# Kernel optimization log

Measured on AMD Instinct MI355X. Metric: run time of the kernel, lower is better.

Reference implementation:

```python
import jax, jax.numpy as jnp
import numpy as np

B, S, D, E, TOPK = 8, 4096, 1024, 64, 2
TEMP = 0.01


def setup_inputs() -> dict:
    key = jax.random.key(0)
    k_x, k_w1, k_b1, k_w2, k_b2 = jax.random.split(key, 5)
    x = jax.random.normal(k_x, (B, S, D), dtype=jnp.float32)
    # torch.nn.Linear default init ~ U(-1/sqrt(fan_in), 1/sqrt(fan_in)); scale ok for reference
    W1 = jax.random.normal(k_w1, (D, 2 * D), dtype=jnp.float32) * (1.0 / np.sqrt(D))
    b1 = jax.random.normal(k_b1, (2 * D,), dtype=jnp.float32) * 0.01
    W2 = jax.random.normal(k_w2, (2 * D, E), dtype=jnp.float32) * (1.0 / np.sqrt(2 * D))
    b2 = jax.random.normal(k_b2, (E,), dtype=jnp.float32) * 0.01
    return {"x": x, "W1": W1, "b1": b1, "W2": W2, "b2": b2}


def reference(x, W1, b1, W2, b2):
    # 2-layer MLP router: [B,S,D] -> [B,S,2D] -> [B,S,E]
    h = jax.nn.relu(jnp.einsum('bsd,df->bsf', x, W1) + b1)
    logits = jnp.einsum('bsf,fe->bse', h, W2) + b2
    # top-k over experts
    top_k_logits, indices = jax.lax.top_k(logits, TOPK)  # [B,S,K]
    # scatter top-k logits into a -inf-filled tensor: equivalent to masking,
    # since scattered values equal logits at those positions
    keep = jax.nn.one_hot(indices, E, dtype=bool).any(axis=-2)  # [B,S,E]
    sparse_logits = jnp.where(keep, logits, -jnp.inf)
    router_output = jax.nn.softmax(sparse_logits, axis=-1)
    ori_router_output = jax.nn.softmax(logits / TEMP, axis=-1)
    return (ori_router_output, router_output, indices)
```

## Files before the change

kernel.cpp:

```cpp
#include <hip/hip_runtime.h>
#include <math.h>
#include <stdint.h>

#define M_TOK 32768
#define D_IN  1024
#define F_HID 2048
#define E_EXP 64

#define O_ORI 0
#define O_RTR (M_TOK * E_EXP)
#define O_IDX (2 * M_TOK * E_EXP)

typedef _Float16 half8 __attribute__((ext_vector_type(8)));
typedef float    f32x4 __attribute__((ext_vector_type(4)));
typedef unsigned int uint32;
typedef uint32   u32x4 __attribute__((ext_vector_type(4)));

#define WS_XH  ((size_t)0)
#define WS_XL  (WS_XH  + (size_t)M_TOK * D_IN * 2)
#define WS_W1H (WS_XL  + (size_t)M_TOK * D_IN * 2)
#define WS_W1L (WS_W1H + (size_t)D_IN * F_HID * 2)
#define WS_W2H (WS_W1L + (size_t)D_IN * F_HID * 2)
#define WS_W2L (WS_W2H + (size_t)F_HID * E_EXP * 2)
#define WS_P   (WS_W2L + (size_t)F_HID * E_EXP * 2)
#define WS_NEED_FULL (WS_P + (size_t)8 * M_TOK * E_EXP * 4)

__device__ __forceinline__ void split_sc(float v, float sc, unsigned short& h, unsigned short& l) {
    const _Float16 hh = (_Float16)v;
    const float hf = (float)hh;
    const _Float16 hs = (_Float16)(hf * sc);
    const _Float16 ls = (_Float16)((v - hf) * sc);
    h = __builtin_bit_cast(unsigned short, hs);
    l = __builtin_bit_cast(unsigned short, ls);
}


__global__ void split_x_k(const float* __restrict__ x,
                          unsigned short* __restrict__ xh, unsigned short* __restrict__ xl) {
    size_t i = ((size_t)blockIdx.x * 256 + threadIdx.x) * 4;
    const float4 v = *(const float4*)&x[i];
    ushort4 h, l;
    split_sc(v.x, 64.f, h.x, l.x); split_sc(v.y, 64.f, h.y, l.y);
    split_sc(v.z, 64.f, h.z, l.z); split_sc(v.w, 64.f, h.w, l.w);
    *(ushort4*)&xh[i] = h;
    *(ushort4*)&xl[i] = l;
}

__global__ void split_w1t_k(const float* __restrict__ W1,
                            unsigned short* __restrict__ wh, unsigned short* __restrict__ wl) {
    __shared__ float t[32][33];
    const int d0 = blockIdx.x * 32;
    const int f0 = blockIdx.y * 32;
    const int r  = threadIdx.x >> 3;
    const int c4 = (threadIdx.x & 7) * 4;
    const float4 v = *(const float4*)&W1[(size_t)(d0 + r) * F_HID + f0 + c4];
    t[r][c4 + 0] = v.x; t[r][c4 + 1] = v.y; t[r][c4 + 2] = v.z; t[r][c4 + 3] = v.w;
    __syncthreads();
    ushort4 h, l;
    split_sc(t[c4 + 0][r], 64.f, h.x, l.x);
    split_sc(t[c4 + 1][r], 64.f, h.y, l.y);
    split_sc(t[c4 + 2][r], 64.f, h.z, l.z);
    split_sc(t[c4 + 3][r], 64.f, h.w, l.w);
    *(ushort4*)&wh[(size_t)(f0 + r) * D_IN + d0 + c4] = h;
    *(ushort4*)&wl[(size_t)(f0 + r) * D_IN + d0 + c4] = l;
}

__global__ void split_w2f_k(const float* __restrict__ W2,
                            unsigned short* __restrict__ wh, unsigned short* __restrict__ wl) {
    const int s  = blockIdx.x;
    const int nt = threadIdx.x >> 6;
    const int l  = threadIdx.x & 63;
    const int fb = s * 32 + (l >> 4) * 8;
    const int e  = nt * 16 + (l & 15);
    unsigned short h[8], lo[8];
#pragma unroll
    for (int j = 0; j < 8; ++j)
        split_sc(W2[(size_t)(fb + j) * E_EXP + e], 16.f, h[j], lo[j]);
    const size_t base = ((size_t)(s * 4 + nt) * 64 + l) * 8;
#pragma unroll
    for (int j = 0; j < 4; ++j) {
        ((ushort4*)&wh[base])[0] = make_ushort4(h[0], h[1], h[2], h[3]);
        ((ushort4*)&wh[base])[1] = make_ushort4(h[4], h[5], h[6], h[7]);
        ((ushort4*)&wl[base])[0] = make_ushort4(lo[0], lo[1], lo[2], lo[3]);
        ((ushort4*)&wl[base])[1] = make_ushort4(lo[4], lo[5], lo[6], lo[7]);
    }
}


__device__ __forceinline__ uint32 swz(uint32 o) { return o ^ (((o >> 7) & 7u) << 4); }

#define STAGE16(SRCP, DSTP) \
    __builtin_amdgcn_global_load_lds((const __attribute__((address_space(1))) void*)(SRCP), \
                                     (__attribute__((address_space(3))) void*)(DSTP), 16, 0, 0)


__launch_bounds__(512, 2)
__global__ void gemm1_8w(const unsigned short* __restrict__ xh, const unsigned short* __restrict__ xl,
                         const unsigned short* __restrict__ w1h, const unsigned short* __restrict__ w1l,
                         const unsigned short* __restrict__ w2fh, const unsigned short* __restrict__ w2fl,
                         const float* __restrict__ b1,
                         float* __restrict__ partials)
{
    __shared__ __align__(16) unsigned char lds[131072];

    const int tid  = threadIdx.x;
    const int lane = tid & 63;
    const int w    = tid >> 6;
    const int c15  = lane & 15;
    const int g    = lane >> 4;
    const int wr   = w >> 2;
    const int wc   = w & 3;

    const int bid  = blockIdx.x;
    const int fblk = bid & 7;
    const int mblk = bid >> 3;
    const size_t tok0 = (size_t)mblk * 128;
    const int f0 = fblk * 256;

    uint32 arow, ahalf, brow[2], bhalf[2];
    {
        const uint32 sA = swz((uint32)(w * 1024 + lane * 16));
        arow = sA >> 6; ahalf = (sA & 63u) >> 1;
#pragma unroll
        for (int j = 0; j < 2; ++j) {
            const uint32 sB = swz((uint32)(j * 8192 + w * 1024 + lane * 16));
            brow[j] = sB >> 6; bhalf[j] = (sB & 63u) >> 1;
        }
    }

    uint32 offA[4], offB[4];
#pragma unroll
    for (int m = 0; m < 4; ++m)
        offA[m] = swz((uint32)((wr * 64 + m * 16 + c15) * 64 + g * 16));
#pragma unroll
    for (int n = 0; n < 4; ++n)
        offB[n] = swz((uint32)((wc * 64 + n * 16 + c15) * 64 + g * 16));

    f32x4 acc[4][4];
#pragma unroll
    for (int m = 0; m < 4; ++m)
#pragma unroll
        for (int n = 0; n < 4; ++n) acc[m][n] = (f32x4){0.f, 0.f, 0.f, 0.f};

#define STAGE_T(T, BUF) do {                                                         \
    const int d0_ = (T) * 32;                                                        \
    const size_t asrc = (tok0 + arow) * D_IN + (size_t)(d0_ + (int)ahalf);           \
    STAGE16(xh + asrc, lds + (BUF) * 16384 + w * 1024);                              \
    STAGE16(xl + asrc, lds + (BUF) * 16384 + 8192 + w * 1024);                       \
    _Pragma("unroll")                                                                \
    for (int j = 0; j < 2; ++j) {                                                    \
        const size_t bsrc = ((size_t)f0 + brow[j]) * D_IN + (size_t)(d0_ + (int)bhalf[j]); \
        STAGE16(w1h + bsrc, lds + 32768 + (BUF) * 32768 + j * 8192 + w * 1024);      \
        STAGE16(w1l + bsrc, lds + 32768 + (BUF) * 32768 + 16384 + j * 8192 + w * 1024); \
    } } while (0)

    STAGE_T(0, 0);
    STAGE_T(1, 1);

#pragma unroll 1
    for (int t = 0; t < 32; ++t) {
        if (t < 31) asm volatile("s_waitcnt vmcnt(6)" ::: "memory");
        else        asm volatile("s_waitcnt vmcnt(0)" ::: "memory");
        __builtin_amdgcn_s_barrier();
        const unsigned char* Ab = lds + (t & 1) * 16384;
        const unsigned char* Bb = lds + 32768 + (t & 1) * 32768;

        half8 b1f[4], b2f[4];
#pragma unroll
        for (int n = 0; n < 4; ++n) {
            b1f[n] = *(const half8*)(Bb + offB[n]);
            b2f[n] = *(const half8*)(Bb + 16384 + offB[n]);
        }
        half8 a1f[2], a2f[2];
#pragma unroll
        for (int m = 0; m < 2; ++m) {
            a1f[m] = *(const half8*)(Ab + offA[m]);
            a2f[m] = *(const half8*)(Ab + 8192 + offA[m]);
        }
        __builtin_amdgcn_s_setprio(1);
#pragma unroll
        for (int m = 0; m < 2; ++m)
#pragma unroll
            for (int n = 0; n < 4; ++n) {
                acc[m][n] = __builtin_amdgcn_mfma_f32_16x16x32_f16(a1f[m], b1f[n], acc[m][n], 0, 0, 0);
                acc[m][n] = __builtin_amdgcn_mfma_f32_16x16x32_f16(a1f[m], b2f[n], acc[m][n], 0, 0, 0);
                acc[m][n] = __builtin_amdgcn_mfma_f32_16x16x32_f16(a2f[m], b1f[n], acc[m][n], 0, 0, 0);
            }
        __builtin_amdgcn_s_setprio(0);
#pragma unroll
        for (int m = 0; m < 2; ++m) {
            a1f[m] = *(const half8*)(Ab + offA[2 + m]);
            a2f[m] = *(const half8*)(Ab + 8192 + offA[2 + m]);
        }
        __builtin_amdgcn_s_setprio(1);
#pragma unroll
        for (int m = 0; m < 2; ++m)
#pragma unroll
            for (int n = 0; n < 4; ++n) {
                acc[2 + m][n] = __builtin_amdgcn_mfma_f32_16x16x32_f16(a1f[m], b1f[n], acc[2 + m][n], 0, 0, 0);
                acc[2 + m][n] = __builtin_amdgcn_mfma_f32_16x16x32_f16(a1f[m], b2f[n], acc[2 + m][n], 0, 0, 0);
                acc[2 + m][n] = __builtin_amdgcn_mfma_f32_16x16x32_f16(a2f[m], b1f[n], acc[2 + m][n], 0, 0, 0);
            }
        __builtin_amdgcn_s_setprio(0);
        __builtin_amdgcn_s_barrier();
        if (t + 2 < 32) STAGE_T(t + 2, t & 1);
    }
#undef STAGE_T

    {
        float bv[4];
#pragma unroll
        for (int n = 0; n < 4; ++n) bv[n] = b1[f0 + wc * 64 + n * 16 + c15];
#pragma unroll
        for (int m = 0; m < 4; ++m)
#pragma unroll
            for (int n = 0; n < 4; ++n)
#pragma unroll
                for (int r = 0; r < 4; ++r) {
                    float hv = acc[m][n][r] * (1.f / 4096.f) + bv[n];
                    hv = fmaxf(hv, 0.f);
                    const _Float16 hh = (_Float16)hv;
                    const float hf = (float)hh;
                    const _Float16 hsv = (_Float16)(hf * 16.f);
                    const _Float16 lsv = (_Float16)((hv - hf) * 16.f);
                    const uint32 pk = (uint32)__builtin_bit_cast(unsigned short, hsv)
                                    | ((uint32)__builtin_bit_cast(unsigned short, lsv) << 16);
                    const int tok = wr * 64 + m * 16 + g * 4 + r;
                    const int fl  = wc * 64 + n * 16 + c15;
                    *(uint32*)(lds + tok * 1024 + ((fl * 4) ^ ((tok & 15) << 4))) = pk;
                }
    }
    __syncthreads();

    f32x4 acc2[4];
#pragma unroll
    for (int nt = 0; nt < 4; ++nt) acc2[nt] = (f32x4){0.f, 0.f, 0.f, 0.f};

    const int wtok0 = w * 16;
    const int tokA  = wtok0 + c15;
#pragma unroll
    for (int s = 0; s < 8; ++s) {
        const int kf = s * 32 + g * 8;
        const int sg = fblk * 8 + s;
        half8 bf1[4], bf2[4];
#pragma unroll
        for (int nt = 0; nt < 4; ++nt) {
            const size_t base = ((size_t)(sg * 4 + nt) * 64 + lane) * 8;
            bf1[nt] = *(const half8*)&w2fh[base];
            bf2[nt] = *(const half8*)&w2fl[base];
        }
        const u32x4 q0 = *(const u32x4*)(lds + tokA * 1024 + (((kf    ) * 4) ^ (c15 << 4)));
        const u32x4 q1 = *(const u32x4*)(lds + tokA * 1024 + (((kf + 4) * 4) ^ (c15 << 4)));
        u32x4 hi4, lo4;
        hi4[0] = __builtin_amdgcn_perm(q0[1], q0[0], 0x05040100u);
        hi4[1] = __builtin_amdgcn_perm(q0[3], q0[2], 0x05040100u);
        hi4[2] = __builtin_amdgcn_perm(q1[1], q1[0], 0x05040100u);
        hi4[3] = __builtin_amdgcn_perm(q1[3], q1[2], 0x05040100u);
        lo4[0] = __builtin_amdgcn_perm(q0[1], q0[0], 0x07060302u);
        lo4[1] = __builtin_amdgcn_perm(q0[3], q0[2], 0x07060302u);
        lo4[2] = __builtin_amdgcn_perm(q1[1], q1[0], 0x07060302u);
        lo4[3] = __builtin_amdgcn_perm(q1[3], q1[2], 0x07060302u);
        const half8 a1 = __builtin_bit_cast(half8, hi4);
        const half8 a2 = __builtin_bit_cast(half8, lo4);
#pragma unroll
        for (int nt = 0; nt < 4; ++nt) {
            acc2[nt] = __builtin_amdgcn_mfma_f32_16x16x32_f16(a1, bf1[nt], acc2[nt], 0, 0, 0);
            acc2[nt] = __builtin_amdgcn_mfma_f32_16x16x32_f16(a1, bf2[nt], acc2[nt], 0, 0, 0);
            acc2[nt] = __builtin_amdgcn_mfma_f32_16x16x32_f16(a2, bf1[nt], acc2[nt], 0, 0, 0);
        }
    }

    float* pout = partials + ((size_t)fblk * M_TOK + tok0) * E_EXP;
#pragma unroll
    for (int nt = 0; nt < 4; ++nt)
#pragma unroll
        for (int r = 0; r < 4; ++r) {
            const int tl = wtok0 + g * 4 + r;
            pout[(size_t)tl * E_EXP + nt * 16 + c15] = acc2[nt][r] * (1.f / 256.f);
        }
}


__launch_bounds__(256, 4)
__global__ void finalize(const float* __restrict__ partials,
                         const float* __restrict__ b2,
                         float* __restrict__ out)
{
    const int lane = threadIdx.x & 63;
    const int w    = threadIdx.x >> 6;
    const size_t tok0 = (size_t)blockIdx.x * 64;
    const int e = lane;
    const float be = b2[e];

#pragma unroll 1
    for (int i = 0; i < 16; ++i) {
        const size_t tok = tok0 + (size_t)w * 16 + i;
        float l = be;
#pragma unroll
        for (int p = 0; p < 8; ++p)
            l += partials[((size_t)p * M_TOK + tok) * E_EXP + e];

        float v = l; int idx = e;
#pragma unroll
        for (int m = 32; m >= 1; m >>= 1) {
            const float ov = __shfl_xor(v, m, 64);
            const int   oi = __shfl_xor(idx, m, 64);
            if (ov > v || (ov == v && oi < idx)) { v = ov; idx = oi; }
        }
        const float m1 = v; const int i1 = idx;

        v = (e == i1) ? -INFINITY : l; idx = e;
#pragma unroll
        for (int m = 32; m >= 1; m >>= 1) {
            const float ov = __shfl_xor(v, m, 64);
            const int   oi = __shfl_xor(idx, m, 64);
            if (ov > v || (ov == v && oi < idx)) { v = ov; idx = oi; }
        }
        const int i2 = idx;

        const float ex = expf((l - m1) * 100.0f);
        float s = ex;
#pragma unroll
        for (int m = 32; m >= 1; m >>= 1) s += __shfl_xor(s, m, 64);
        const float ori = ex / s;

        const float q = (e == i1 || e == i2) ? expf(l - m1) : 0.f;
        float s2 = q;
#pragma unroll
        for (int m = 32; m >= 1; m >>= 1) s2 += __shfl_xor(s2, m, 64);
        const float rtr = q / s2;

        out[O_ORI + tok * E_EXP + e] = ori;
        out[O_RTR + tok * E_EXP + e] = rtr;
        if (e == 0) {
            out[O_IDX + tok * 2 + 0] = (float)i1;
            out[O_IDX + tok * 2 + 1] = (float)i2;
        }
    }
}


#define BT  64
#define NB  256

__launch_bounds__(256, 2)
__global__ void router_mfma(const unsigned short* __restrict__ xh, const unsigned short* __restrict__ xl,
                            const unsigned short* __restrict__ w1h, const unsigned short* __restrict__ w1l,
                            const unsigned short* __restrict__ w2fh, const unsigned short* __restrict__ w2fl,
                            const float* __restrict__ b1, const float* __restrict__ b2,
                            float* __restrict__ out)
{
    __shared__ __align__(16) unsigned char xs_h[BT * 64];
    __shared__ __align__(16) unsigned char xs_l[BT * 64];
    __shared__ __align__(16) unsigned char w1s_h[NB * 64];
    __shared__ __align__(16) unsigned char w1s_l[NB * 64];
    __shared__ __align__(16) unsigned char hsbuf[BT * 132 * 4];

    const int tid  = threadIdx.x;
    const int lane = tid & 63;
    const int w    = tid >> 6;
    const int c15  = lane & 15;
    const int g    = lane >> 4;
    const size_t tok0 = (size_t)blockIdx.x * BT;

    uint32* hs = (uint32*)hsbuf;
    float*  ls = (float*)hsbuf;

    f32x4 acc2h[4], acc2x[4];
#pragma unroll
    for (int nt = 0; nt < 4; ++nt) {
        acc2h[nt] = (f32x4){0.f, 0.f, 0.f, 0.f};
        acc2x[nt] = (f32x4){0.f, 0.f, 0.f, 0.f};
    }

    const uint32 kqb = (uint32)g * 16u;

    for (int fc = 0; fc < F_HID; fc += NB) {
        f32x4 ahh[4][4], axx[4][4];
#pragma unroll
        for (int mt = 0; mt < 4; ++mt)
#pragma unroll
            for (int nt = 0; nt < 4; ++nt) {
                ahh[mt][nt] = (f32x4){0.f, 0.f, 0.f, 0.f};
                axx[mt][nt] = (f32x4){0.f, 0.f, 0.f, 0.f};
            }

        for (int d0 = 0; d0 < D_IN; d0 += 32) {
            __syncthreads();
            {
                uint32 o = (uint32)w * 1024u + (uint32)lane * 16u;
                uint32 s = swz(o);
                uint32 r = s >> 6, hb = (s & 63u) >> 1;
                const unsigned short* sp;
                sp = xh + (tok0 + r) * D_IN + (size_t)(d0 + (int)hb);
                STAGE16(sp, xs_h + (size_t)w * 1024);
                sp = xl + (tok0 + r) * D_IN + (size_t)(d0 + (int)hb);
                STAGE16(sp, xs_l + (size_t)w * 1024);
#pragma unroll
                for (int q = 0; q < 4; ++q) {
                    const uint32 c_ = (uint32)(q * 4 + w);
                    uint32 o2 = c_ * 1024u + (uint32)lane * 16u;
                    uint32 s2 = swz(o2);
                    uint32 r2 = s2 >> 6, hb2 = (s2 & 63u) >> 1;
                    sp = w1h + ((size_t)(fc + (int)r2)) * D_IN + (size_t)(d0 + (int)hb2);
                    STAGE16(sp, w1s_h + (size_t)c_ * 1024);
                    sp = w1l + ((size_t)(fc + (int)r2)) * D_IN + (size_t)(d0 + (int)hb2);
                    STAGE16(sp, w1s_l + (size_t)c_ * 1024);
                }
            }
            __syncthreads();

            half8 ah[4], al[4], bh[4], bl[4];
#pragma unroll
            for (int mt = 0; mt < 4; ++mt) {
                const uint32 off = swz((uint32)(mt * 16 + c15) * 64u + kqb);
                ah[mt] = *(const half8*)(xs_h + off);
                al[mt] = *(const half8*)(xs_l + off);
            }
#pragma unroll
            for (int nt = 0; nt < 4; ++nt) {
                const uint32 row = (uint32)(w * 64 + nt * 16 + c15);
                const uint32 off = swz(row * 64u + kqb);
                bh[nt] = *(const half8*)(w1s_h + off);
                bl[nt] = *(const half8*)(w1s_l + off);
            }
#pragma unroll
            for (int mt = 0; mt < 4; ++mt)
#pragma unroll
                for (int nt = 0; nt < 4; ++nt) {
                    ahh[mt][nt] = __builtin_amdgcn_mfma_f32_16x16x32_f16(ah[mt], bh[nt], ahh[mt][nt], 0, 0, 0);
                    axx[mt][nt] = __builtin_amdgcn_mfma_f32_16x16x32_f16(ah[mt], bl[nt], axx[mt][nt], 0, 0, 0);
                    axx[mt][nt] = __builtin_amdgcn_mfma_f32_16x16x32_f16(al[mt], bh[nt], axx[mt][nt], 0, 0, 0);
                }
        }

        const int fl0 = (w & 1) * 64;
#pragma unroll
        for (int phase = 0; phase < 2; ++phase) {
            if ((w >> 1) == phase) {
#pragma unroll
                for (int nt = 0; nt < 4; ++nt) {
                    const float b1v = b1[fc + w * 64 + nt * 16 + c15];
#pragma unroll
                    for (int mt = 0; mt < 4; ++mt) {
#pragma unroll
                        for (int r = 0; r < 4; ++r) {
                            float hv = (ahh[mt][nt][r] + axx[mt][nt][r]) * (1.f / 4096.f) + b1v;
                            hv = fmaxf(hv, 0.f);
                            const _Float16 hhv0 = (_Float16)hv;
                            const float hf = (float)hhv0;
                            const _Float16 hhv = (_Float16)(hf * 16.f);
                            const _Float16 hlv = (_Float16)((hv - hf) * 16.f);
                            uint32 pk = (uint32)__builtin_bit_cast(unsigned short, hhv)
                                      | ((uint32)__builtin_bit_cast(unsigned short, hlv) << 16);
                            const int t = mt * 16 + g * 4 + r;
                            hs[t * 132 + fl0 + nt * 16 + c15] = pk;
                        }
                    }
                }
            }
            __syncthreads();
            const int tA = w * 16 + c15;
#pragma unroll
            for (int ktl = 0; ktl < 4; ++ktl) {
                const u32x4 q0 = *(const u32x4*)&hs[tA * 132 + ktl * 32 + g * 8];
                const u32x4 q1 = *(const u32x4*)&hs[tA * 132 + ktl * 32 + g * 8 + 4];
                u32x4 hi4, lo4;
                hi4[0] = __builtin_amdgcn_perm(q0[1], q0[0], 0x05040100u);
                hi4[1] = __builtin_amdgcn_perm(q0[3], q0[2], 0x05040100u);
                hi4[2] = __builtin_amdgcn_perm(q1[1], q1[0], 0x05040100u);
                hi4[3] = __builtin_amdgcn_perm(q1[3], q1[2], 0x05040100u);
                lo4[0] = __builtin_amdgcn_perm(q0[1], q0[0], 0x07060302u);
                lo4[1] = __builtin_amdgcn_perm(q0[3], q0[2], 0x07060302u);
                lo4[2] = __builtin_amdgcn_perm(q1[1], q1[0], 0x07060302u);
                lo4[3] = __builtin_amdgcn_perm(q1[3], q1[2], 0x07060302u);
                const half8 a_h = __builtin_bit_cast(half8, hi4);
                const half8 a_l = __builtin_bit_cast(half8, lo4);
                const int sg = (fc >> 5) + phase * 4 + ktl;
#pragma unroll
                for (int nt = 0; nt < 4; ++nt) {
                    const size_t base = ((size_t)(sg * 4 + nt) * 64 + lane) * 8;
                    const half8 b_h = *(const half8*)&w2fh[base];
                    const half8 b_l = *(const half8*)&w2fl[base];
                    acc2h[nt] = __builtin_amdgcn_mfma_f32_16x16x32_f16(a_h, b_h, acc2h[nt], 0, 0, 0);
                    acc2x[nt] = __builtin_amdgcn_mfma_f32_16x16x32_f16(a_h, b_l, acc2x[nt], 0, 0, 0);
                    acc2x[nt] = __builtin_amdgcn_mfma_f32_16x16x32_f16(a_l, b_h, acc2x[nt], 0, 0, 0);
                }
            }
            __syncthreads();
        }
    }

#pragma unroll
    for (int nt = 0; nt < 4; ++nt)
#pragma unroll
        for (int r = 0; r < 4; ++r) {
            const int t = w * 16 + g * 4 + r;
            ls[t * 68 + nt * 16 + c15] = (acc2h[nt][r] + acc2x[nt][r]) * (1.f / 256.f);
        }
    __syncthreads();

    const int e = lane;
    const float be = b2[e];
#pragma unroll 1
    for (int i = 0; i < 16; ++i) {
        const float l = ls[(w * 16 + i) * 68 + e] + be;

        float v = l; int idx = e;
#pragma unroll
        for (int m = 32; m >= 1; m >>= 1) {
            const float ov = __shfl_xor(v, m, 64);
            const int   oi = __shfl_xor(idx, m, 64);
            if (ov > v || (ov == v && oi < idx)) { v = ov; idx = oi; }
        }
        const float m1 = v; const int i1 = idx;

        v = (e == i1) ? -INFINITY : l; idx = e;
#pragma unroll
        for (int m = 32; m >= 1; m >>= 1) {
            const float ov = __shfl_xor(v, m, 64);
            const int   oi = __shfl_xor(idx, m, 64);
            if (ov > v || (ov == v && oi < idx)) { v = ov; idx = oi; }
        }
        const int i2 = idx;

        const float ex = expf((l - m1) * 100.0f);
        float s = ex;
#pragma unroll
        for (int m = 32; m >= 1; m >>= 1) s += __shfl_xor(s, m, 64);
        const float ori = ex / s;

        const float q = (e == i1 || e == i2) ? expf(l - m1) : 0.f;
        float s2 = q;
#pragma unroll
        for (int m = 32; m >= 1; m >>= 1) s2 += __shfl_xor(s2, m, 64);
        const float rtr = q / s2;

        const size_t tok = tok0 + (size_t)w * 16 + i;
        out[O_ORI + tok * E_EXP + e] = ori;
        out[O_RTR + tok * E_EXP + e] = rtr;
        if (e == 0) {
            out[O_IDX + tok * 2 + 0] = (float)i1;
            out[O_IDX + tok * 2 + 1] = (float)i2;
        }
    }
}


extern "C" void kernel_launch(void* const* d_in, const int* in_sizes, int n_in,
                              void* d_out, int out_size, void* d_ws, size_t ws_size,
                              hipStream_t stream) {
    const float* x  = (const float*)d_in[0];
    const float* W1 = (const float*)d_in[1];
    const float* b1 = (const float*)d_in[2];
    const float* W2 = (const float*)d_in[3];
    const float* b2 = (const float*)d_in[4];
    float* out = (float*)d_out;

    unsigned char* ws = (unsigned char*)d_ws;
    unsigned short* xh  = (unsigned short*)(ws + WS_XH);
    unsigned short* xl  = (unsigned short*)(ws + WS_XL);
    unsigned short* w1h = (unsigned short*)(ws + WS_W1H);
    unsigned short* w1l = (unsigned short*)(ws + WS_W1L);
    unsigned short* w2h = (unsigned short*)(ws + WS_W2H);
    unsigned short* w2l = (unsigned short*)(ws + WS_W2L);
    float*          parts = (float*)(ws + WS_P);

    hipLaunchKernelGGL(split_x_k,  dim3(M_TOK * D_IN / 4 / 256), dim3(256), 0, stream, x, xh, xl);
    hipLaunchKernelGGL(split_w1t_k, dim3(D_IN / 32, F_HID / 32), dim3(256), 0, stream, W1, w1h, w1l);
    hipLaunchKernelGGL(split_w2f_k, dim3(F_HID / 32), dim3(256), 0, stream, W2, w2h, w2l);

    if (ws_size >= WS_NEED_FULL) {
        hipLaunchKernelGGL(gemm1_8w, dim3(2048), dim3(512), 0, stream,
                           xh, xl, w1h, w1l, w2h, w2l, b1, parts);
        hipLaunchKernelGGL(finalize, dim3(M_TOK / 64), dim3(256), 0, stream, parts, b2, out);
    } else {
        hipLaunchKernelGGL(router_mfma, dim3(M_TOK / BT), dim3(256), 0, stream,
                           xh, xl, w1h, w1l, w2h, w2l, b1, b2, out);
    }
}
```

Baseline: 528.0 us.

## Split fused GEMM into two hidden halves to halve LDS and double occupancy

The fused GEMM1+GEMM2 kernel now handles its 256 hidden columns as two sequential 128-column halves. Each half runs the K loop, writes relu(h) to LDS and folds it into the GEMM2 accumulator, so LDS drops from 128 KB to 64 KB, the accumulator tile halves, and launch bounds request 4 blocks per CU instead of 2. The aim is more resident waves to hide latency, at the cost of loading the x tile twice and adding extra barriers per block. A redundant 4x repeated store loop in the W2 split kernel is also removed.

```diff
diff --git a/kernel.cpp b/kernel.cpp
--- a/kernel.cpp
+++ b/kernel.cpp
@@ -77,13 +77,10 @@
     for (int j = 0; j < 8; ++j)
         split_sc(W2[(size_t)(fb + j) * E_EXP + e], 16.f, h[j], lo[j]);
     const size_t base = ((size_t)(s * 4 + nt) * 64 + l) * 8;
-#pragma unroll
-    for (int j = 0; j < 4; ++j) {
-        ((ushort4*)&wh[base])[0] = make_ushort4(h[0], h[1], h[2], h[3]);
-        ((ushort4*)&wh[base])[1] = make_ushort4(h[4], h[5], h[6], h[7]);
-        ((ushort4*)&wl[base])[0] = make_ushort4(lo[0], lo[1], lo[2], lo[3]);
-        ((ushort4*)&wl[base])[1] = make_ushort4(lo[4], lo[5], lo[6], lo[7]);
-    }
+    ((ushort4*)&wh[base])[0] = make_ushort4(h[0], h[1], h[2], h[3]);
+    ((ushort4*)&wh[base])[1] = make_ushort4(h[4], h[5], h[6], h[7]);
+    ((ushort4*)&wl[base])[0] = make_ushort4(lo[0], lo[1], lo[2], lo[3]);
+    ((ushort4*)&wl[base])[1] = make_ushort4(lo[4], lo[5], lo[6], lo[7]);
 }
 
 
@@ -94,14 +91,14 @@
                                      (__attribute__((address_space(3))) void*)(DSTP), 16, 0, 0)
 
 
-__launch_bounds__(512, 2)
+__launch_bounds__(512, 4)
 __global__ void gemm1_8w(const unsigned short* __restrict__ xh, const unsigned short* __restrict__ xl,
                          const unsigned short* __restrict__ w1h, const unsigned short* __restrict__ w1l,
                          const unsigned short* __restrict__ w2fh, const unsigned short* __restrict__ w2fl,
                          const float* __restrict__ b1,
                          float* __restrict__ partials)
 {
-    __shared__ __align__(16) unsigned char lds[131072];
+    __shared__ __align__(16) unsigned char lds[65536];
 
     const int tid  = threadIdx.x;
     const int lane = tid & 63;
@@ -109,7 +106,7 @@
     const int c15  = lane & 15;
     const int g    = lane >> 4;
     const int wr   = w >> 2;
-    const int wc   = w & 3;
+    const int wcq  = w & 3;
 
     const int bid  = blockIdx.x;
     const int fblk = bid & 7;
@@ -117,165 +114,165 @@
     const size_t tok0 = (size_t)mblk * 128;
     const int f0 = fblk * 256;
 
-    uint32 arow, ahalf, brow[2], bhalf[2];
+    uint32 srow, shalf;
     {
-        const uint32 sA = swz((uint32)(w * 1024 + lane * 16));
-        arow = sA >> 6; ahalf = (sA & 63u) >> 1;
-#pragma unroll
-        for (int j = 0; j < 2; ++j) {
-            const uint32 sB = swz((uint32)(j * 8192 + w * 1024 + lane * 16));
-            brow[j] = sB >> 6; bhalf[j] = (sB & 63u) >> 1;
-        }
-    }
-
-    uint32 offA[4], offB[4];
+        const uint32 s_ = swz((uint32)(tid * 16));
+        srow = s_ >> 6; shalf = (s_ & 63u) >> 1;
+    }
+
+    uint32 offA[4], offB[2];
 #pragma unroll
     for (int m = 0; m < 4; ++m)
         offA[m] = swz((uint32)((wr * 64 + m * 16 + c15) * 64 + g * 16));
 #pragma unroll
-    for (int n = 0; n < 4; ++n)
-        offB[n] = swz((uint32)((wc * 64 + n * 16 + c15) * 64 + g * 16));
-
-    f32x4 acc[4][4];
-#pragma unroll
-    for (int m = 0; m < 4; ++m)
-#pragma unroll
-        for (int n = 0; n < 4; ++n) acc[m][n] = (f32x4){0.f, 0.f, 0.f, 0.f};
+    for (int n = 0; n < 2; ++n)
+        offB[n] = swz((uint32)((wcq * 32 + n * 16 + c15) * 64 + g * 16));
+
+    f32x4 acc2[4];
+#pragma unroll
+    for (int nt = 0; nt < 4; ++nt) acc2[nt] = (f32x4){0.f, 0.f, 0.f, 0.f};
 
 #define STAGE_T(T, BUF) do {                                                         \
     const int d0_ = (T) * 32;                                                        \
-    const size_t asrc = (tok0 + arow) * D_IN + (size_t)(d0_ + (int)ahalf);           \
-    STAGE16(xh + asrc, lds + (BUF) * 16384 + w * 1024);                              \
-    STAGE16(xl + asrc, lds + (BUF) * 16384 + 8192 + w * 1024);                       \
-    _Pragma("unroll")                                                                \
-    for (int j = 0; j < 2; ++j) {                                                    \
-        const size_t bsrc = ((size_t)f0 + brow[j]) * D_IN + (size_t)(d0_ + (int)bhalf[j]); \
-        STAGE16(w1h + bsrc, lds + 32768 + (BUF) * 32768 + j * 8192 + w * 1024);      \
-        STAGE16(w1l + bsrc, lds + 32768 + (BUF) * 32768 + 16384 + j * 8192 + w * 1024); \
-    } } while (0)
-
-    STAGE_T(0, 0);
-    STAGE_T(1, 1);
+    const size_t asrc = (tok0 + srow) * D_IN + (size_t)(d0_ + (int)shalf);           \
+    const size_t bsrc = ((size_t)fh + srow) * D_IN + (size_t)(d0_ + (int)shalf);     \
+    STAGE16(xh  + asrc, lds + (BUF) * 16384 + w * 1024);                             \
+    STAGE16(xl  + asrc, lds + (BUF) * 16384 + 8192 + w * 1024);                      \
+    STAGE16(w1h + bsrc, lds + 32768 + (BUF) * 16384 + w * 1024);                     \
+    STAGE16(w1l + bsrc, lds + 32768 + (BUF) * 16384 + 8192 + w * 1024);              \
+} while (0)
 
 #pragma unroll 1
-    for (int t = 0; t < 32; ++t) {
-        if (t < 31) asm volatile("s_waitcnt vmcnt(6)" ::: "memory");
-        else        asm volatile("s_waitcnt vmcnt(0)" ::: "memory");
-        __builtin_amdgcn_s_barrier();
-        const unsigned char* Ab = lds + (t & 1) * 16384;
-        const unsigned char* Bb = lds + 32768 + (t & 1) * 32768;
-
-        half8 b1f[4], b2f[4];
-#pragma unroll
-        for (int n = 0; n < 4; ++n) {
-            b1f[n] = *(const half8*)(Bb + offB[n]);
-            b2f[n] = *(const half8*)(Bb + 16384 + offB[n]);
-        }
-        half8 a1f[2], a2f[2];
-#pragma unroll
-        for (int m = 0; m < 2; ++m) {
-            a1f[m] = *(const half8*)(Ab + offA[m]);
-            a2f[m] = *(const half8*)(Ab + 8192 + offA[m]);
-        }
-        __builtin_amdgcn_s_setprio(1);
-#pragma unroll
-        for (int m = 0; m < 2; ++m)
-#pragma unroll
-            for (int n = 0; n < 4; ++n) {
-                acc[m][n] = __builtin_amdgcn_mfma_f32_16x16x32_f16(a1f[m], b1f[n], acc[m][n], 0, 0, 0);
-                acc[m][n] = __builtin_amdgcn_mfma_f32_16x16x32_f16(a1f[m], b2f[n], acc[m][n], 0, 0, 0);
-                acc[m][n] = __builtin_amdgcn_mfma_f32_16x16x32_f16(a2f[m], b1f[n], acc[m][n], 0, 0, 0);
-            }
-        __builtin_amdgcn_s_setprio(0);
-#pragma unroll
-        for (int m = 0; m < 2; ++m) {
-            a1f[m] = *(const half8*)(Ab + offA[2 + m]);
-            a2f[m] = *(const half8*)(Ab + 8192 + offA[2 + m]);
-        }
-        __builtin_amdgcn_s_setprio(1);
-#pragma unroll
-        for (int m = 0; m < 2; ++m)
-#pragma unroll
-            for (int n = 0; n < 4; ++n) {
-                acc[2 + m][n] = __builtin_amdgcn_mfma_f32_16x16x32_f16(a1f[m], b1f[n], acc[2 + m][n], 0, 0, 0);
-                acc[2 + m][n] = __builtin_amdgcn_mfma_f32_16x16x32_f16(a1f[m], b2f[n], acc[2 + m][n], 0, 0, 0);
-                acc[2 + m][n] = __builtin_amdgcn_mfma_f32_16x16x32_f16(a2f[m], b1f[n], acc[2 + m][n], 0, 0, 0);
-            }
-        __builtin_amdgcn_s_setprio(0);
-        __builtin_amdgcn_s_barrier();
-        if (t + 2 < 32) STAGE_T(t + 2, t & 1);
+    for (int half = 0; half < 2; ++half) {
+        const int fh = f0 + half * 128;
+
+        f32x4 acc[4][2];
+#pragma unroll
+        for (int m = 0; m < 4; ++m)
+#pragma unroll
+            for (int n = 0; n < 2; ++n) acc[m][n] = (f32x4){0.f, 0.f, 0.f, 0.f};
+
+        STAGE_T(0, 0);
+        STAGE_T(1, 1);
+
+#pragma unroll 1
+        for (int t = 0; t < 32; ++t) {
+            if (t < 31) asm volatile("s_waitcnt vmcnt(4)" ::: "memory");
+            else        asm volatile("s_waitcnt vmcnt(0)" ::: "memory");
+            __builtin_amdgcn_s_barrier();
+            const unsigned char* Ab = lds + (t & 1) * 16384;
+            const unsigned char* Bb = lds + 32768 + (t & 1) * 16384;
+
+            half8 b1f[2], b2f[2];
+#pragma unroll
+            for (int n = 0; n < 2; ++n) {
+                b1f[n] = *(const half8*)(Bb + offB[n]);
+                b2f[n] = *(const half8*)(Bb + 8192 + offB[n]);
+            }
+            half8 a1f[2], a2f[2];
+#pragma unroll
+            for (int m = 0; m < 2; ++m) {
+                a1f[m] = *(const half8*)(Ab + offA[m]);
+                a2f[m] = *(const half8*)(Ab + 8192 + offA[m]);
+            }
+            __builtin_amdgcn_s_setprio(1);
+#pragma unroll
+            for (int m = 0; m < 2; ++m)
+#pragma unroll
+                for (int n = 0; n < 2; ++n) {
+                    acc[m][n] = __builtin_amdgcn_mfma_f32_16x16x32_f16(a1f[m], b1f[n], acc[m][n], 0, 0, 0);
+                    acc[m][n] = __builtin_amdgcn_mfma_f32_16x16x32_f16(a1f[m], b2f[n], acc[m][n], 0, 0, 0);
+                    acc[m][n] = __builtin_amdgcn_mfma_f32_16x16x32_f16(a2f[m], b1f[n], acc[m][n], 0, 0, 0);
+                }
+            __builtin_amdgcn_s_setprio(0);
+#pragma unroll
+            for (int m = 0; m < 2; ++m) {
+                a1f[m] = *(const half8*)(Ab + offA[2 + m]);
+                a2f[m] = *(const half8*)(Ab + 8192 + offA[2 + m]);
+            }
+            __builtin_amdgcn_s_setprio(1);
+#pragma unroll
+            for (int m = 0; m < 2; ++m)
+#pragma unroll
+                for (int n = 0; n < 2; ++n) {
+                    acc[2 + m][n] = __builtin_amdgcn_mfma_f32_16x16x32_f16(a1f[m], b1f[n], acc[2 + m][n], 0, 0, 0);
+                    acc[2 + m][n] = __builtin_amdgcn_mfma_f32_16x16x32_f16(a1f[m], b2f[n], acc[2 + m][n], 0, 0, 0);
+                    acc[2 + m][n] = __builtin_amdgcn_mfma_f32_16x16x32_f16(a2f[m], b1f[n], acc[2 + m][n], 0, 0, 0);
+                }
+            __builtin_amdgcn_s_setprio(0);
+            __builtin_amdgcn_s_barrier();
+            if (t + 2 < 32) STAGE_T(t + 2, t & 1);
+        }
+
+        {
+            float bv[2];
+#pragma unroll
+            for (int n = 0; n < 2; ++n) bv[n] = b1[fh + wcq * 32 + n * 16 + c15];
+#pragma unroll
+            for (int m = 0; m < 4; ++m)
+#pragma unroll
+                for (int n = 0; n < 2; ++n)
+#pragma unroll
+                    for (int r = 0; r < 4; ++r) {
+                        float hv = acc[m][n][r] * (1.f / 4096.f) + bv[n];
+                        hv = fmaxf(hv, 0.f);
+                        const _Float16 hh = (_Float16)hv;
+                        const float hf = (float)hh;
+                        const _Float16 hsv = (_Float16)(hf * 16.f);
+                        const _Float16 lsv = (_Float16)((hv - hf) * 16.f);
+                        const uint32 pk = (uint32)__builtin_bit_cast(unsigned short, hsv)
+                                        | ((uint32)__builtin_bit_cast(unsigned short, lsv) << 16);
+                        const int tok = wr * 64 + m * 16 + g * 4 + r;
+                        const int fl  = wcq * 32 + n * 16 + c15;
+                        *(uint32*)(lds + tok * 512 + ((fl * 4) ^ ((tok & 15) << 4))) = pk;
+                    }
+        }
+        __syncthreads();
+
+        {
+            const int tokA = w * 16 + c15;
+#pragma unroll
+            for (int s = 0; s < 4; ++s) {
+                const int kf = s * 32 + g * 8;
+                const int sg = (fh >> 5) + s;
+                half8 bf1[4], bf2[4];
+#pragma unroll
+                for (int nt = 0; nt < 4; ++nt) {
+                    const size_t base = ((size_t)(sg * 4 + nt) * 64 + lane) * 8;
+                    bf1[nt] = *(const half8*)&w2fh[base];
+                    bf2[nt] = *(const half8*)&w2fl[base];
+                }
+                const u32x4 q0 = *(const u32x4*)(lds + tokA * 512 + (((kf    ) * 4) ^ ((tokA & 15) << 4)));
+                const u32x4 q1 = *(const u32x4*)(lds + tokA * 512 + (((kf + 4) * 4) ^ ((tokA & 15) << 4)));
+                u32x4 hi4, lo4;
+                hi4[0] = __builtin_amdgcn_perm(q0[1], q0[0], 0x05040100u);
+                hi4[1] = __builtin_amdgcn_perm(q0[3], q0[2], 0x05040100u);
+                hi4[2] = __builtin_amdgcn_perm(q1[1], q1[0], 0x05040100u);
+                hi4[3] = __builtin_amdgcn_perm(q1[3], q1[2], 0x05040100u);
+                lo4[0] = __builtin_amdgcn_perm(q0[1], q0[0], 0x07060302u);
+                lo4[1] = __builtin_amdgcn_perm(q0[3], q0[2], 0x07060302u);
+                lo4[2] = __builtin_amdgcn_perm(q1[1], q1[0], 0x07060302u);
+                lo4[3] = __builtin_amdgcn_perm(q1[3], q1[2], 0x07060302u);
+                const half8 a1 = __builtin_bit_cast(half8, hi4);
+                const half8 a2 = __builtin_bit_cast(half8, lo4);
+#pragma unroll
+                for (int nt = 0; nt < 4; ++nt) {
+                    acc2[nt] = __builtin_amdgcn_mfma_f32_16x16x32_f16(a1, bf1[nt], acc2[nt], 0, 0, 0);
+                    acc2[nt] = __builtin_amdgcn_mfma_f32_16x16x32_f16(a1, bf2[nt], acc2[nt], 0, 0, 0);
+                    acc2[nt] = __builtin_amdgcn_mfma_f32_16x16x32_f16(a2, bf1[nt], acc2[nt], 0, 0, 0);
+                }
+            }
+        }
+        __syncthreads();
     }
 #undef STAGE_T
 
-    {
-        float bv[4];
-#pragma unroll
-        for (int n = 0; n < 4; ++n) bv[n] = b1[f0 + wc * 64 + n * 16 + c15];
-#pragma unroll
-        for (int m = 0; m < 4; ++m)
-#pragma unroll
-            for (int n = 0; n < 4; ++n)
-#pragma unroll
-                for (int r = 0; r < 4; ++r) {
-                    float hv = acc[m][n][r] * (1.f / 4096.f) + bv[n];
-                    hv = fmaxf(hv, 0.f);
-                    const _Float16 hh = (_Float16)hv;
-                    const float hf = (float)hh;
-                    const _Float16 hsv = (_Float16)(hf * 16.f);
-                    const _Float16 lsv = (_Float16)((hv - hf) * 16.f);
-                    const uint32 pk = (uint32)__builtin_bit_cast(unsigned short, hsv)
-                                    | ((uint32)__builtin_bit_cast(unsigned short, lsv) << 16);
-                    const int tok = wr * 64 + m * 16 + g * 4 + r;
-                    const int fl  = wc * 64 + n * 16 + c15;
-                    *(uint32*)(lds + tok * 1024 + ((fl * 4) ^ ((tok & 15) << 4))) = pk;
-                }
-    }
-    __syncthreads();
-
-    f32x4 acc2[4];
-#pragma unroll
-    for (int nt = 0; nt < 4; ++nt) acc2[nt] = (f32x4){0.f, 0.f, 0.f, 0.f};
-
-    const int wtok0 = w * 16;
-    const int tokA  = wtok0 + c15;
-#pragma unroll
-    for (int s = 0; s < 8; ++s) {
-        const int kf = s * 32 + g * 8;
-        const int sg = fblk * 8 + s;
-        half8 bf1[4], bf2[4];
-#pragma unroll
-        for (int nt = 0; nt < 4; ++nt) {
-            const size_t base = ((size_t)(sg * 4 + nt) * 64 + lane) * 8;
-            bf1[nt] = *(const half8*)&w2fh[base];
-            bf2[nt] = *(const half8*)&w2fl[base];
-        }
-        const u32x4 q0 = *(const u32x4*)(lds + tokA * 1024 + (((kf    ) * 4) ^ (c15 << 4)));
-        const u32x4 q1 = *(const u32x4*)(lds + tokA * 1024 + (((kf + 4) * 4) ^ (c15 << 4)));
-        u32x4 hi4, lo4;
-        hi4[0] = __builtin_amdgcn_perm(q0[1], q0[0], 0x05040100u);
-        hi4[1] = __builtin_amdgcn_perm(q0[3], q0[2], 0x05040100u);
-        hi4[2] = __builtin_amdgcn_perm(q1[1], q1[0], 0x05040100u);
-        hi4[3] = __builtin_amdgcn_perm(q1[3], q1[2], 0x05040100u);
-        lo4[0] = __builtin_amdgcn_perm(q0[1], q0[0], 0x07060302u);
-        lo4[1] = __builtin_amdgcn_perm(q0[3], q0[2], 0x07060302u);
-        lo4[2] = __builtin_amdgcn_perm(q1[1], q1[0], 0x07060302u);
-        lo4[3] = __builtin_amdgcn_perm(q1[3], q1[2], 0x07060302u);
-        const half8 a1 = __builtin_bit_cast(half8, hi4);
-        const half8 a2 = __builtin_bit_cast(half8, lo4);
-#pragma unroll
-        for (int nt = 0; nt < 4; ++nt) {
-            acc2[nt] = __builtin_amdgcn_mfma_f32_16x16x32_f16(a1, bf1[nt], acc2[nt], 0, 0, 0);
-            acc2[nt] = __builtin_amdgcn_mfma_f32_16x16x32_f16(a1, bf2[nt], acc2[nt], 0, 0, 0);
-            acc2[nt] = __builtin_amdgcn_mfma_f32_16x16x32_f16(a2, bf1[nt], acc2[nt], 0, 0, 0);
-        }
-    }
-
     float* pout = partials + ((size_t)fblk * M_TOK + tok0) * E_EXP;
 #pragma unroll
     for (int nt = 0; nt < 4; ++nt)
 #pragma unroll
         for (int r = 0; r < 4; ++r) {
-            const int tl = wtok0 + g * 4 + r;
+            const int tl = w * 16 + g * 4 + r;
             pout[(size_t)tl * E_EXP + nt * 16 + c15] = acc2[nt][r] * (1.f / 256.f);
         }
 }
```

New measurement: 555.1 us. 5.1% more time.

## Double GEMM1 token tile to 256 and split second GEMM into two rounds

Applied to the files above, without the earlier changes.

Each block of the fused GEMM kernel now covers 256 tokens instead of 128, halving the grid and doubling per-wave accumulators, so every W1 tile staged into LDS serves twice as many tokens. The next-stage prefetch is issued partway through the inner loop, after the second half of the A fragments is loaded, to overlap loads with MFMA work. The relu/split-to-LDS step and the W2 GEMM now run in two rounds of 128 tokens, reusing the LDS buffer. It also removes a redundant 4x repeated store loop in the W2 split kernel. The costs are higher register pressure (32 accumulator tiles) under launch_bounds(512,2) and fewer blocks to fill the GPU.

```diff
diff --git a/kernel.cpp b/kernel.cpp
--- a/kernel.cpp
+++ b/kernel.cpp
@@ -77,13 +77,10 @@
     for (int j = 0; j < 8; ++j)
         split_sc(W2[(size_t)(fb + j) * E_EXP + e], 16.f, h[j], lo[j]);
     const size_t base = ((size_t)(s * 4 + nt) * 64 + l) * 8;
-#pragma unroll
-    for (int j = 0; j < 4; ++j) {
-        ((ushort4*)&wh[base])[0] = make_ushort4(h[0], h[1], h[2], h[3]);
-        ((ushort4*)&wh[base])[1] = make_ushort4(h[4], h[5], h[6], h[7]);
-        ((ushort4*)&wl[base])[0] = make_ushort4(lo[0], lo[1], lo[2], lo[3]);
-        ((ushort4*)&wl[base])[1] = make_ushort4(lo[4], lo[5], lo[6], lo[7]);
-    }
+    ((ushort4*)&wh[base])[0] = make_ushort4(h[0], h[1], h[2], h[3]);
+    ((ushort4*)&wh[base])[1] = make_ushort4(h[4], h[5], h[6], h[7]);
+    ((ushort4*)&wl[base])[0] = make_ushort4(lo[0], lo[1], lo[2], lo[3]);
+    ((ushort4*)&wl[base])[1] = make_ushort4(lo[4], lo[5], lo[6], lo[7]);
 }
 
 
@@ -114,44 +111,42 @@
     const int bid  = blockIdx.x;
     const int fblk = bid & 7;
     const int mblk = bid >> 3;
-    const size_t tok0 = (size_t)mblk * 128;
+    const size_t tok0 = (size_t)mblk * 256;
     const int f0 = fblk * 256;
 
-    uint32 arow, ahalf, brow[2], bhalf[2];
-    {
-        const uint32 sA = swz((uint32)(w * 1024 + lane * 16));
-        arow = sA >> 6; ahalf = (sA & 63u) >> 1;
-#pragma unroll
-        for (int j = 0; j < 2; ++j) {
-            const uint32 sB = swz((uint32)(j * 8192 + w * 1024 + lane * 16));
-            brow[j] = sB >> 6; bhalf[j] = (sB & 63u) >> 1;
-        }
-    }
-
-    uint32 offA[4], offB[4];
-#pragma unroll
-    for (int m = 0; m < 4; ++m)
-        offA[m] = swz((uint32)((wr * 64 + m * 16 + c15) * 64 + g * 16));
+    uint32 srow[2], shalf[2];
+#pragma unroll
+    for (int j = 0; j < 2; ++j) {
+        const uint32 c_ = (uint32)(w + 8 * j);
+        const uint32 s_ = swz(c_ * 1024u + (uint32)lane * 16u);
+        srow[j] = s_ >> 6; shalf[j] = (s_ & 63u) >> 1;
+    }
+
+    uint32 offA[8], offB[4];
+#pragma unroll
+    for (int m = 0; m < 8; ++m)
+        offA[m] = swz((uint32)(wr * 128 + m * 16 + c15) * 64u + (uint32)g * 16u);
 #pragma unroll
     for (int n = 0; n < 4; ++n)
-        offB[n] = swz((uint32)((wc * 64 + n * 16 + c15) * 64 + g * 16));
-
-    f32x4 acc[4][4];
-#pragma unroll
-    for (int m = 0; m < 4; ++m)
+        offB[n] = swz((uint32)(wc * 64 + n * 16 + c15) * 64u + (uint32)g * 16u);
+
+    f32x4 acc[8][4];
+#pragma unroll
+    for (int m = 0; m < 8; ++m)
 #pragma unroll
         for (int n = 0; n < 4; ++n) acc[m][n] = (f32x4){0.f, 0.f, 0.f, 0.f};
 
-#define STAGE_T(T, BUF) do {                                                         \
-    const int d0_ = (T) * 32;                                                        \
-    const size_t asrc = (tok0 + arow) * D_IN + (size_t)(d0_ + (int)ahalf);           \
-    STAGE16(xh + asrc, lds + (BUF) * 16384 + w * 1024);                              \
-    STAGE16(xl + asrc, lds + (BUF) * 16384 + 8192 + w * 1024);                       \
-    _Pragma("unroll")                                                                \
-    for (int j = 0; j < 2; ++j) {                                                    \
-        const size_t bsrc = ((size_t)f0 + brow[j]) * D_IN + (size_t)(d0_ + (int)bhalf[j]); \
-        STAGE16(w1h + bsrc, lds + 32768 + (BUF) * 32768 + j * 8192 + w * 1024);      \
-        STAGE16(w1l + bsrc, lds + 32768 + (BUF) * 32768 + 16384 + j * 8192 + w * 1024); \
+#define STAGE_T(T, BUF) do {                                                        \
+    const int d0_ = (T) * 32;                                                       \
+    _Pragma("unroll")                                                               \
+    for (int j = 0; j < 2; ++j) {                                                   \
+        const uint32 c_ = (uint32)(w + 8 * j);                                      \
+        const size_t asrc = (tok0 + srow[j]) * D_IN + (size_t)(d0_ + (int)shalf[j]);\
+        const size_t bsrc = ((size_t)(f0) + srow[j]) * D_IN + (size_t)(d0_ + (int)shalf[j]); \
+        STAGE16(xh  + asrc, lds + (BUF) * 32768 + c_ * 1024);                       \
+        STAGE16(xl  + asrc, lds + (BUF) * 32768 + 16384 + c_ * 1024);               \
+        STAGE16(w1h + bsrc, lds + 65536 + (BUF) * 32768 + c_ * 1024);               \
+        STAGE16(w1l + bsrc, lds + 65536 + (BUF) * 32768 + 16384 + c_ * 1024);       \
     } } while (0)
 
     STAGE_T(0, 0);
@@ -159,11 +154,11 @@
 
 #pragma unroll 1
     for (int t = 0; t < 32; ++t) {
-        if (t < 31) asm volatile("s_waitcnt vmcnt(6)" ::: "memory");
+        if (t < 31) asm volatile("s_waitcnt vmcnt(8)" ::: "memory");
         else        asm volatile("s_waitcnt vmcnt(0)" ::: "memory");
         __builtin_amdgcn_s_barrier();
-        const unsigned char* Ab = lds + (t & 1) * 16384;
-        const unsigned char* Bb = lds + 32768 + (t & 1) * 32768;
+        const unsigned char* Ab = lds + (t & 1) * 32768;
+        const unsigned char* Bb = lds + 65536 + (t & 1) * 32768;
 
         half8 b1f[4], b2f[4];
 #pragma unroll
@@ -171,15 +166,15 @@
             b1f[n] = *(const half8*)(Bb + offB[n]);
             b2f[n] = *(const half8*)(Bb + 16384 + offB[n]);
         }
-        half8 a1f[2], a2f[2];
-#pragma unroll
-        for (int m = 0; m < 2; ++m) {
+        half8 a1f[4], a2f[4];
+#pragma unroll
+        for (int m = 0; m < 4; ++m) {
             a1f[m] = *(const half8*)(Ab + offA[m]);
-            a2f[m] = *(const half8*)(Ab + 8192 + offA[m]);
+            a2f[m] = *(const half8*)(Ab + 16384 + offA[m]);
         }
         __builtin_amdgcn_s_setprio(1);
 #pragma unroll
-        for (int m = 0; m < 2; ++m)
+        for (int m = 0; m < 4; ++m)
 #pragma unroll
             for (int n = 0; n < 4; ++n) {
                 acc[m][n] = __builtin_amdgcn_mfma_f32_16x16x32_f16(a1f[m], b1f[n], acc[m][n], 0, 0, 0);
@@ -187,97 +182,106 @@
                 acc[m][n] = __builtin_amdgcn_mfma_f32_16x16x32_f16(a2f[m], b1f[n], acc[m][n], 0, 0, 0);
             }
         __builtin_amdgcn_s_setprio(0);
-#pragma unroll
-        for (int m = 0; m < 2; ++m) {
-            a1f[m] = *(const half8*)(Ab + offA[2 + m]);
-            a2f[m] = *(const half8*)(Ab + 8192 + offA[2 + m]);
-        }
-        __builtin_amdgcn_s_setprio(1);
-#pragma unroll
-        for (int m = 0; m < 2; ++m)
-#pragma unroll
-            for (int n = 0; n < 4; ++n) {
-                acc[2 + m][n] = __builtin_amdgcn_mfma_f32_16x16x32_f16(a1f[m], b1f[n], acc[2 + m][n], 0, 0, 0);
-                acc[2 + m][n] = __builtin_amdgcn_mfma_f32_16x16x32_f16(a1f[m], b2f[n], acc[2 + m][n], 0, 0, 0);
-                acc[2 + m][n] = __builtin_amdgcn_mfma_f32_16x16x32_f16(a2f[m], b1f[n], acc[2 + m][n], 0, 0, 0);
-            }
-        __builtin_amdgcn_s_setprio(0);
+        half8 c1f[4], c2f[4];
+#pragma unroll
+        for (int m = 0; m < 4; ++m) {
+            c1f[m] = *(const half8*)(Ab + offA[4 + m]);
+            c2f[m] = *(const half8*)(Ab + 16384 + offA[4 + m]);
+        }
+        asm volatile("s_waitcnt lgkmcnt(0)" ::: "memory");
         __builtin_amdgcn_s_barrier();
         if (t + 2 < 32) STAGE_T(t + 2, t & 1);
+        __builtin_amdgcn_s_setprio(1);
+#pragma unroll
+        for (int m = 0; m < 4; ++m)
+#pragma unroll
+            for (int n = 0; n < 4; ++n) {
+                acc[4 + m][n] = __builtin_amdgcn_mfma_f32_16x16x32_f16(c1f[m], b1f[n], acc[4 + m][n], 0, 0, 0);
+                acc[4 + m][n] = __builtin_amdgcn_mfma_f32_16x16x32_f16(c1f[m], b2f[n], acc[4 + m][n], 0, 0, 0);
+                acc[4 + m][n] = __builtin_amdgcn_mfma_f32_16x16x32_f16(c2f[m], b1f[n], acc[4 + m][n], 0, 0, 0);
+            }
+        __builtin_amdgcn_s_setprio(0);
     }
 #undef STAGE_T
 
-    {
-        float bv[4];
-#pragma unroll
-        for (int n = 0; n < 4; ++n) bv[n] = b1[f0 + wc * 64 + n * 16 + c15];
-#pragma unroll
-        for (int m = 0; m < 4; ++m)
-#pragma unroll
-            for (int n = 0; n < 4; ++n)
-#pragma unroll
-                for (int r = 0; r < 4; ++r) {
-                    float hv = acc[m][n][r] * (1.f / 4096.f) + bv[n];
-                    hv = fmaxf(hv, 0.f);
-                    const _Float16 hh = (_Float16)hv;
-                    const float hf = (float)hh;
-                    const _Float16 hsv = (_Float16)(hf * 16.f);
-                    const _Float16 lsv = (_Float16)((hv - hf) * 16.f);
-                    const uint32 pk = (uint32)__builtin_bit_cast(unsigned short, hsv)
-                                    | ((uint32)__builtin_bit_cast(unsigned short, lsv) << 16);
-                    const int tok = wr * 64 + m * 16 + g * 4 + r;
-                    const int fl  = wc * 64 + n * 16 + c15;
-                    *(uint32*)(lds + tok * 1024 + ((fl * 4) ^ ((tok & 15) << 4))) = pk;
-                }
-    }
     __syncthreads();
 
-    f32x4 acc2[4];
-#pragma unroll
-    for (int nt = 0; nt < 4; ++nt) acc2[nt] = (f32x4){0.f, 0.f, 0.f, 0.f};
-
-    const int wtok0 = w * 16;
-    const int tokA  = wtok0 + c15;
-#pragma unroll
-    for (int s = 0; s < 8; ++s) {
-        const int kf = s * 32 + g * 8;
-        const int sg = fblk * 8 + s;
-        half8 bf1[4], bf2[4];
-#pragma unroll
-        for (int nt = 0; nt < 4; ++nt) {
-            const size_t base = ((size_t)(sg * 4 + nt) * 64 + lane) * 8;
-            bf1[nt] = *(const half8*)&w2fh[base];
-            bf2[nt] = *(const half8*)&w2fl[base];
-        }
-        const u32x4 q0 = *(const u32x4*)(lds + tokA * 1024 + (((kf    ) * 4) ^ (c15 << 4)));
-        const u32x4 q1 = *(const u32x4*)(lds + tokA * 1024 + (((kf + 4) * 4) ^ (c15 << 4)));
-        u32x4 hi4, lo4;
-        hi4[0] = __builtin_amdgcn_perm(q0[1], q0[0], 0x05040100u);
-        hi4[1] = __builtin_amdgcn_perm(q0[3], q0[2], 0x05040100u);
-        hi4[2] = __builtin_amdgcn_perm(q1[1], q1[0], 0x05040100u);
-        hi4[3] = __builtin_amdgcn_perm(q1[3], q1[2], 0x05040100u);
-        lo4[0] = __builtin_amdgcn_perm(q0[1], q0[0], 0x07060302u);
-        lo4[1] = __builtin_amdgcn_perm(q0[3], q0[2], 0x07060302u);
-        lo4[2] = __builtin_amdgcn_perm(q1[1], q1[0], 0x07060302u);
-        lo4[3] = __builtin_amdgcn_perm(q1[3], q1[2], 0x07060302u);
-        const half8 a1 = __builtin_bit_cast(half8, hi4);
-        const half8 a2 = __builtin_bit_cast(half8, lo4);
-#pragma unroll
-        for (int nt = 0; nt < 4; ++nt) {
-            acc2[nt] = __builtin_amdgcn_mfma_f32_16x16x32_f16(a1, bf1[nt], acc2[nt], 0, 0, 0);
-            acc2[nt] = __builtin_amdgcn_mfma_f32_16x16x32_f16(a1, bf2[nt], acc2[nt], 0, 0, 0);
-            acc2[nt] = __builtin_amdgcn_mfma_f32_16x16x32_f16(a2, bf1[nt], acc2[nt], 0, 0, 0);
-        }
-    }
+    float bv[4];
+#pragma unroll
+    for (int n = 0; n < 4; ++n) bv[n] = b1[f0 + wc * 64 + n * 16 + c15];
 
     float* pout = partials + ((size_t)fblk * M_TOK + tok0) * E_EXP;
-#pragma unroll
-    for (int nt = 0; nt < 4; ++nt)
-#pragma unroll
-        for (int r = 0; r < 4; ++r) {
-            const int tl = wtok0 + g * 4 + r;
-            pout[(size_t)tl * E_EXP + nt * 16 + c15] = acc2[nt][r] * (1.f / 256.f);
-        }
+
+#pragma unroll 1
+    for (int round = 0; round < 2; ++round) {
+        if (wr == round) {
+#pragma unroll
+            for (int m = 0; m < 8; ++m)
+#pragma unroll
+                for (int n = 0; n < 4; ++n)
+#pragma unroll
+                    for (int r = 0; r < 4; ++r) {
+                        float hv = acc[m][n][r] * (1.f / 4096.f) + bv[n];
+                        hv = fmaxf(hv, 0.f);
+                        const _Float16 hh = (_Float16)hv;
+                        const float hf = (float)hh;
+                        const _Float16 hsv = (_Float16)(hf * 16.f);
+                        const _Float16 lsv = (_Float16)((hv - hf) * 16.f);
+                        const uint32 pk = (uint32)__builtin_bit_cast(unsigned short, hsv)
+                                        | ((uint32)__builtin_bit_cast(unsigned short, lsv) << 16);
+                        const int tok = m * 16 + g * 4 + r;
+                        const int fl  = wc * 64 + n * 16 + c15;
+                        *(uint32*)(lds + tok * 1024 + ((fl * 4) ^ ((tok & 15) << 4))) = pk;
+                    }
+        }
+        __syncthreads();
+
+        f32x4 acc2[4];
+#pragma unroll
+        for (int nt = 0; nt < 4; ++nt) acc2[nt] = (f32x4){0.f, 0.f, 0.f, 0.f};
+
+        const int tokA = w * 16 + c15;
+#pragma unroll
+        for (int s = 0; s < 8; ++s) {
+            const int kf = s * 32 + g * 8;
+            const int sg = fblk * 8 + s;
+            half8 bf1[4], bf2[4];
+#pragma unroll
+            for (int nt = 0; nt < 4; ++nt) {
+                const size_t base = ((size_t)(sg * 4 + nt) * 64 + lane) * 8;
+                bf1[nt] = *(const half8*)&w2fh[base];
+                bf2[nt] = *(const half8*)&w2fl[base];
+            }
+            const u32x4 q0 = *(const u32x4*)(lds + tokA * 1024 + (((kf    ) * 4) ^ ((tokA & 15) << 4)));
+            const u32x4 q1 = *(const u32x4*)(lds + tokA * 1024 + (((kf + 4) * 4) ^ ((tokA & 15) << 4)));
+            u32x4 hi4, lo4;
+            hi4[0] = __builtin_amdgcn_perm(q0[1], q0[0], 0x05040100u);
+            hi4[1] = __builtin_amdgcn_perm(q0[3], q0[2], 0x05040100u);
+            hi4[2] = __builtin_amdgcn_perm(q1[1], q1[0], 0x05040100u);
+            hi4[3] = __builtin_amdgcn_perm(q1[3], q1[2], 0x05040100u);
+            lo4[0] = __builtin_amdgcn_perm(q0[1], q0[0], 0x07060302u);
+            lo4[1] = __builtin_amdgcn_perm(q0[3], q0[2], 0x07060302u);
+            lo4[2] = __builtin_amdgcn_perm(q1[1], q1[0], 0x07060302u);
+            lo4[3] = __builtin_amdgcn_perm(q1[3], q1[2], 0x07060302u);
+            const half8 a1 = __builtin_bit_cast(half8, hi4);
+            const half8 a2 = __builtin_bit_cast(half8, lo4);
+#pragma unroll
+            for (int nt = 0; nt < 4; ++nt) {
+                acc2[nt] = __builtin_amdgcn_mfma_f32_16x16x32_f16(a1, bf1[nt], acc2[nt], 0, 0, 0);
+                acc2[nt] = __builtin_amdgcn_mfma_f32_16x16x32_f16(a1, bf2[nt], acc2[nt], 0, 0, 0);
+                acc2[nt] = __builtin_amdgcn_mfma_f32_16x16x32_f16(a2, bf1[nt], acc2[nt], 0, 0, 0);
+            }
+        }
+
+#pragma unroll
+        for (int nt = 0; nt < 4; ++nt)
+#pragma unroll
+            for (int r = 0; r < 4; ++r) {
+                const int tl = round * 128 + w * 16 + g * 4 + r;
+                pout[(size_t)tl * E_EXP + nt * 16 + c15] = acc2[nt][r] * (1.f / 256.f);
+            }
+        __syncthreads();
+    }
 }
 
 
@@ -571,7 +575,7 @@
     hipLaunchKernelGGL(split_w2f_k, dim3(F_HID / 32), dim3(256), 0, stream, W2, w2h, w2l);
 
     if (ws_size >= WS_NEED_FULL) {
-        hipLaunchKernelGGL(gemm1_8w, dim3(2048), dim3(512), 0, stream,
+        hipLaunchKernelGGL(gemm1_8w, dim3(1024), dim3(512), 0, stream,
                            xh, xl, w1h, w1l, w2h, w2l, b1, parts);
         hipLaunchKernelGGL(finalize, dim3(M_TOK / 64), dim3(256), 0, stream, parts, b2, out);
     } else {
```

Result: slower. 795.5 us (+50.7%).
